# Optimization experiments

Hardware: AMD Instinct MI355X
Metric: run time of the kernel (lower is better)

## Reference

```python
import jax, jax.numpy as jnp
import numpy as np

L, H, LATENT, DM, DH, FF = 4, 4, 256, 768, 192, 1024
EPS = 1e-6      # fast_transformers RecurrentLinearAttention eps
LN_EPS = 1e-5


def make_pe(d_model=LATENT, max_len=5000):
    pos = np.arange(max_len, dtype=np.float32)[:, None]
    div = np.exp(np.arange(0, d_model, 2, dtype=np.float32) * (-np.log(10000.0) / d_model))
    pe = np.zeros((max_len, d_model), np.float32)
    pe[:, 0::2] = np.sin(pos * div)
    pe[:, 1::2] = np.cos(pos * div)
    return jnp.asarray(pe)

PE = make_pe()


def layer_norm(x, g, b):
    m = x.mean(-1, keepdims=True)
    v = ((x - m) ** 2).mean(-1, keepdims=True)
    return (x - m) * jax.lax.rsqrt(v + LN_EPS) * g + b


def setup_inputs() -> dict:
    key = jax.random.key(0)
    ks = jax.random.split(key, 16)
    bs, nj, nf, T, A, C = 8, 25, 6, 80, 6, 12
    s = 0.02
    return dict(
        x=jax.random.normal(ks[0], (bs, nj, nf, T), jnp.float32),
        y=jax.random.randint(ks[1], (bs, A), 0, C),
        ind_map=jnp.sort(jax.random.randint(ks[2], (T, bs), 0, A), axis=0),
        act_tstamps=jnp.sort(jax.random.randint(ks[3], (bs, A), 1, T + 1), axis=1).at[:, -1].set(T),
        skel_W=jax.random.normal(ks[4], (nj * nf, LATENT), jnp.float32) * s,
        skel_b=jnp.zeros((LATENT,), jnp.float32),
        muQuery=jax.random.normal(ks[5], (C, LATENT), jnp.float32),
        sigmaQuery=jax.random.normal(ks[6], (C, LATENT), jnp.float32),
        Wq=jax.random.normal(ks[7], (L, DM, DM), jnp.float32) * s,
        bq=jnp.zeros((L, DM), jnp.float32),
        Wk=jax.random.normal(ks[8], (L, DM, DM), jnp.float32) * s,
        bk=jnp.zeros((L, DM), jnp.float32),
        Wv=jax.random.normal(ks[9], (L, DM, DM), jnp.float32) * s,
        bv=jnp.zeros((L, DM), jnp.float32),
        Wo=jax.random.normal(ks[10], (L, DM, DM), jnp.float32) * s,
        bo=jnp.zeros((L, DM), jnp.float32),
        W1=jax.random.normal(ks[11], (L, DM, FF), jnp.float32) * s,
        b1=jnp.zeros((L, FF), jnp.float32),
        W2=jax.random.normal(ks[12], (L, FF, DM), jnp.float32) * s,
        b2=jnp.zeros((L, DM), jnp.float32),
        ln1_g=jnp.ones((L, DM), jnp.float32), ln1_b=jnp.zeros((L, DM), jnp.float32),
        ln2_g=jnp.ones((L, DM), jnp.float32), ln2_b=jnp.zeros((L, DM), jnp.float32),
        lnf_g=jnp.ones((DM,), jnp.float32), lnf_b=jnp.zeros((DM,), jnp.float32),
    )


def _fwd(x, y, ind_map, act_tstamps, skel_W, skel_b, muQuery, sigmaQuery,
         Wq, bq, Wk, bk, Wv, bv, Wo, bo, W1, b1, W2, b2,
         ln1_g, ln1_b, ln2_g, ln2_b, lnf_g, lnf_b):
    bs, nj, nf, T = x.shape
    # skeleton embedding: [T, bs, njoints*nfeats] @ W -> [T, bs, LATENT]
    xe = x.transpose(3, 0, 1, 2).reshape(T, bs, nj * nf) @ skel_W + skel_b
    mu_q = muQuery[y]        # [bs, A, LATENT]
    sig_q = sigmaQuery[y]
    barange = jnp.arange(bs)

    @jax.checkpoint
    def step(carry, inputs):
        S, Z = carry                         # [L,bs,H,DH,DH], [L,bs,H,DH]
        t, xt, ind_t = inputs
        cm = mu_q[barange, ind_t]            # gather per-sample current action query
        cs = sig_q[barange, ind_t]
        xseq = jnp.stack([cm, cs, xt], 0)    # [3, bs, LATENT]
        start = jnp.where(t == 0, 0, t + 2)  # PositionalEncoding(last_pos=t, offset=2)
        pe3 = jax.lax.dynamic_slice_in_dim(PE, start, 3, 0)
        xseq = xseq + pe3[:, None, :]
        h = xseq.transpose(1, 0, 2).reshape(bs, 3 * LATENT)  # flatten -> [bs, DM]
        nS, nZ = [], []
        for l in range(L):
            q = (h @ Wq[l] + bq[l]).reshape(bs, H, DH)
            k = (h @ Wk[l] + bk[l]).reshape(bs, H, DH)
            v = (h @ Wv[l] + bv[l]).reshape(bs, H, DH)
            Q = jax.nn.elu(q) + 1.0          # linear-attention feature map
            K = jax.nn.elu(k) + 1.0
            Sl = S[l] + K[..., :, None] * v[..., None, :]   # state update S += k (x) v
            Zl = Z[l] + K
            inv = 1.0 / (jnp.einsum('bhd,bhd->bh', Q, Zl) + EPS)
            att = jnp.einsum('bhd,bhdm,bh->bhm', Q, Sl, inv).reshape(bs, DM)
            h1 = layer_norm(h + att @ Wo[l] + bo[l], ln1_g[l], ln1_b[l])
            ffn = jax.nn.relu(h1 @ W1[l] + b1[l]) @ W2[l] + b2[l]
            h = layer_norm(h1 + ffn, ln2_g[l], ln2_b[l])
            nS.append(Sl); nZ.append(Zl)
        h = layer_norm(h, lnf_g, lnf_b)      # encoder final norm
        return (jnp.stack(nS), jnp.stack(nZ)), h

    S0 = jnp.zeros((L, bs, H, DH, DH), x.dtype)
    Z0 = jnp.zeros((L, bs, H, DH), x.dtype)
    _, finals = jax.lax.scan(step, (S0, Z0), (jnp.arange(T), xe, ind_map))  # finals: [T,bs,DM]
    tsel = jnp.maximum(act_tstamps - 1, 0)                       # [bs, A]
    mu = finals[:, :, :LATENT][tsel, barange[:, None]]           # [bs, A, LATENT]
    logvar = finals[:, :, LATENT:2 * LATENT][tsel, barange[:, None]]
    return mu, logvar


def reference(x, y, ind_map, act_tstamps, skel_W, skel_b, muQuery, sigmaQuery,
              Wq, bq, Wk, bk, Wv, bv, Wo, bo, W1, b1, W2, b2,
              ln1_g, ln1_b, ln2_g, ln2_b, lnf_g, lnf_b):
    return _fwd(x, y, ind_map, act_tstamps, skel_W, skel_b, muQuery, sigmaQuery,
                Wq, bq, Wk, bk, Wv, bv, Wo, bo, W1, b1, W2, b2,
                ln1_g, ln1_b, ln2_g, ln2_b, lnf_g, lnf_b)
```

## Files before the change

### kernel.cpp

```cpp
#include <hip/hip_runtime.h>
#include <math.h>

#define TT 80
#define BS 8
#define NA 6
#define DMODEL 768
#define NH 4
#define DH 192
#define FFD 1024
#define NROWS (TT*BS)
#define NQKV (3*DMODEL)

typedef __bf16 bf16;
typedef __bf16 bf16x8 __attribute__((ext_vector_type(8)));
typedef float  f32x4  __attribute__((ext_vector_type(4)));

__device__ __forceinline__ float block_reduce_sum256(float v, float* sm4) {
#pragma unroll
    for (int off = 32; off > 0; off >>= 1) v += __shfl_down(v, off, 64);
    int lane = threadIdx.x & 63, wid = threadIdx.x >> 6;
    if (lane == 0) sm4[wid] = v;
    __syncthreads();
    float r = sm4[0] + sm4[1] + sm4[2] + sm4[3];
    __syncthreads();
    return r;
}

__global__ __launch_bounds__(256) void embed_k(
        const float* __restrict__ x, const int* __restrict__ y,
        const int* __restrict__ ind_map, const float* __restrict__ skel_W,
        const float* __restrict__ skel_b, const float* __restrict__ muQ,
        const float* __restrict__ sigQ, float* __restrict__ h0,
        bf16* __restrict__ h0b) {
    __shared__ float xrow[152];
    int r = blockIdx.x;
    int t = r >> 3, b = r & 7;
    int c = threadIdx.x;
    if (c < 150) xrow[c] = x[(b * 150 + c) * TT + t];
    __syncthreads();
    float acc = skel_b[c];
    for (int jf = 0; jf < 150; jf++) acc += xrow[jf] * skel_W[jf * 256 + c];
    int ind_t = ind_map[t * 8 + b];
    int yb = y[b * NA + ind_t];
    float cm = muQ[yb * 256 + c];
    float cs = sigQ[yb * 256 + c];
    int start = (t == 0) ? 0 : (t + 2);
    float div = expf((float)(c & ~1) * (-9.210340371976184f / 256.0f));
    float p0, p1, p2;
    if (c & 1) {
        p0 = cosf((float)start * div);
        p1 = cosf((float)(start + 1) * div);
        p2 = cosf((float)(start + 2) * div);
    } else {
        p0 = sinf((float)start * div);
        p1 = sinf((float)(start + 1) * div);
        p2 = sinf((float)(start + 2) * div);
    }
    float* hr = h0 + (size_t)r * DMODEL;
    float v0 = cm + p0, v1 = cs + p1, v2 = acc + p2;
    hr[c] = v0; hr[c + 256] = v1; hr[c + 512] = v2;
    bf16* hb = h0b + (size_t)r * DMODEL;
    hb[c] = (bf16)v0; hb[c + 256] = (bf16)v1; hb[c + 512] = (bf16)v2;
}

__global__ __launch_bounds__(256) void transpose_k(
        const float* __restrict__ wq, const float* __restrict__ wk,
        const float* __restrict__ wv, const float* __restrict__ wo,
        const float* __restrict__ w1, const float* __restrict__ w2,
        bf16* __restrict__ qkvT, bf16* __restrict__ woT,
        bf16* __restrict__ w1T, bf16* __restrict__ w2T) {
    int z = blockIdx.z;
    int K = (z == 3) ? 1024 : 768;
    int N = (z == 0) ? 2304 : (z == 2) ? 1024 : 768;
    int k0 = blockIdx.x * 32, n0 = blockIdx.y * 32;
    if (k0 >= K || n0 >= N) return;
    const float* src; bf16* dst; int ldsrc; int ncol;
    if (z == 0) {
        if (n0 < 768)       { src = wq; ncol = n0; }
        else if (n0 < 1536) { src = wk; ncol = n0 - 768; }
        else                { src = wv; ncol = n0 - 1536; }
        dst = qkvT; ldsrc = 768;
    } else if (z == 1) { src = wo; dst = woT; ldsrc = 768;  ncol = n0; }
    else if (z == 2)   { src = w1; dst = w1T; ldsrc = 1024; ncol = n0; }
    else               { src = w2; dst = w2T; ldsrc = 768;  ncol = n0; }
    __shared__ float tile[32][33];
    int tx = threadIdx.x & 31, ty = threadIdx.x >> 5;
#pragma unroll
    for (int i = 0; i < 4; i++) {
        int r = ty + 8 * i;
        tile[r][tx] = src[(size_t)(k0 + r) * ldsrc + ncol + tx];
    }
    __syncthreads();
#pragma unroll
    for (int i = 0; i < 4; i++) {
        int r = ty + 8 * i;
        dst[(size_t)(n0 + r) * K + k0 + tx] = (bf16)tile[tx][r];
    }
}

template <int EPI>
__global__ __launch_bounds__(256) void gemm_mfma(
        const bf16* __restrict__ A, const bf16* __restrict__ Bt,
        const float* __restrict__ bias_q, const float* __restrict__ bias_k,
        const float* __restrict__ bias_v, const float* __restrict__ resid,
        float* __restrict__ outF, bf16* __restrict__ outB,
        int M, int N, int K) {
    __shared__ __attribute__((aligned(16))) bf16 As[64][40];
    __shared__ __attribute__((aligned(16))) bf16 Bs[64][40];
    int tid = threadIdx.x;
    int m0 = blockIdx.y * 64, n0 = blockIdx.x * 64;
    int w = tid >> 6;
    int l = tid & 63;
    int lm = l & 15, lq = l >> 4;
    int sr = tid >> 2;
    int sk = (tid & 3) * 8;
    f32x4 acc[4] = {};
    for (int k0 = 0; k0 < K; k0 += 32) {
        uint4 av = *(const uint4*)&A[(size_t)(m0 + sr) * K + k0 + sk];
        uint4 bv = *(const uint4*)&Bt[(size_t)(n0 + sr) * K + k0 + sk];
        __syncthreads();
        *(uint4*)&As[sr][sk] = av;
        *(uint4*)&Bs[sr][sk] = bv;
        __syncthreads();
        bf16x8 af = *(bf16x8*)&As[w * 16 + lm][lq * 8];
#pragma unroll
        for (int nb = 0; nb < 4; nb++) {
            bf16x8 bfr = *(bf16x8*)&Bs[nb * 16 + lm][lq * 8];
            acc[nb] = __builtin_amdgcn_mfma_f32_16x16x32_bf16(af, bfr, acc[nb], 0, 0, 0);
        }
    }
#pragma unroll
    for (int nb = 0; nb < 4; nb++) {
        int col = n0 + nb * 16 + lm;
        float b;
        bool do_elu = false;
        if (EPI == 0) {
            if (col < 768)       { b = bias_q[col];        do_elu = true; }
            else if (col < 1536) { b = bias_k[col - 768];  do_elu = true; }
            else                 { b = bias_v[col - 1536]; }
        } else {
            b = bias_q[col];
        }
#pragma unroll
        for (int r = 0; r < 4; r++) {
            int row = m0 + w * 16 + lq * 4 + r;
            float v = acc[nb][r] + b;
            if (EPI == 0) {
                if (do_elu) v = (v > 0.0f) ? (v + 1.0f) : expf(v);
                outB[(size_t)row * N + col] = (bf16)v;
            } else if (EPI == 1) {
                v += resid[(size_t)row * N + col];
                outF[(size_t)row * N + col] = v;
            } else {
                v = fmaxf(v, 0.0f);
                outB[(size_t)row * N + col] = (bf16)v;
            }
        }
    }
}

__global__ __launch_bounds__(256) void ln_k(
        const float* __restrict__ in, float* __restrict__ outF,
        bf16* __restrict__ outB,
        const float* __restrict__ g, const float* __restrict__ b) {
    __shared__ float sm4[4];
    int row = blockIdx.x;
    const float* xr = in + (size_t)row * DMODEL;
    int c = threadIdx.x;
    float x0 = xr[c], x1 = xr[c + 256], x2 = xr[c + 512];
    float m = block_reduce_sum256(x0 + x1 + x2, sm4) * (1.0f / 768.0f);
    float d0 = x0 - m, d1 = x1 - m, d2 = x2 - m;
    float v = block_reduce_sum256(d0 * d0 + d1 * d1 + d2 * d2, sm4) * (1.0f / 768.0f);
    float r = rsqrtf(v + 1e-5f);
    float o0 = d0 * r * g[c] + b[c];
    float o1 = d1 * r * g[c + 256] + b[c + 256];
    float o2 = d2 * r * g[c + 512] + b[c + 512];
    float* orow = outF + (size_t)row * DMODEL;
    orow[c] = o0; orow[c + 256] = o1; orow[c + 512] = o2;
    bf16* brow = outB + (size_t)row * DMODEL;
    brow[c] = (bf16)o0; brow[c + 256] = (bf16)o1; brow[c + 512] = (bf16)o2;
}

__global__ __launch_bounds__(320) void attn_k(
        const bf16* __restrict__ qkvB, bf16* __restrict__ att) {
    __shared__ __attribute__((aligned(16))) char smem[64000];
    bf16* Qs = (bf16*)smem;
    bf16* Ks = (bf16*)(smem + 32000);
    bf16* Aij = (bf16*)smem;
    bf16* VT = (bf16*)(smem + 16640);

    int b = blockIdx.x >> 2, h = blockIdx.x & 3;
    int tid = threadIdx.x;
    int w = tid >> 6, l = tid & 63;
    int lm = l & 15, lq = l >> 4;

    uint4 vreg[6];
#pragma unroll
    for (int u = 0; u < 6; u++) {
        int c = tid + 320 * u;
        int t = c / 24, cc = c % 24;
        int d0 = cc * 8;
        size_t g = (size_t)(t * 8 + b) * NQKV + h * DH + d0;
        uint4 qv = *(const uint4*)&qkvB[g];
        uint4 kv = *(const uint4*)&qkvB[g + 768];
        vreg[u]  = *(const uint4*)&qkvB[g + 1536];
        *(uint4*)&Qs[t * 200 + d0] = qv;
        *(uint4*)&Ks[t * 200 + d0] = kv;
    }
    __syncthreads();

    f32x4 acc[5] = {};
#pragma unroll
    for (int k0 = 0; k0 < 192; k0 += 32) {
        bf16x8 af = *(bf16x8*)&Qs[(w * 16 + lm) * 200 + lq * 8 + k0];
#pragma unroll
        for (int nb = 0; nb < 5; nb++) {
            bf16x8 bfr = *(bf16x8*)&Ks[(nb * 16 + lm) * 200 + lq * 8 + k0];
            acc[nb] = __builtin_amdgcn_mfma_f32_16x16x32_bf16(af, bfr, acc[nb], 0, 0, 0);
        }
    }
    float mval[5][4];
    float rs[4] = {0.f, 0.f, 0.f, 0.f};
#pragma unroll
    for (int nb = 0; nb < 5; nb++)
#pragma unroll
        for (int r = 0; r < 4; r++) {
            int t = w * 16 + lq * 4 + r, tau = nb * 16 + lm;
            float v = (tau <= t) ? acc[nb][r] : 0.0f;
            mval[nb][r] = v;
            rs[r] += v;
        }
#pragma unroll
    for (int mk = 1; mk < 16; mk <<= 1)
#pragma unroll
        for (int r = 0; r < 4; r++) rs[r] += __shfl_xor(rs[r], mk, 64);
    float inv[4];
#pragma unroll
    for (int r = 0; r < 4; r++) inv[r] = 1.0f / (rs[r] + 1e-6f);

    __syncthreads();

#pragma unroll
    for (int nb = 0; nb < 5; nb++)
#pragma unroll
        for (int r = 0; r < 4; r++)
            Aij[(w * 16 + lq * 4 + r) * 104 + nb * 16 + lm] = (bf16)mval[nb][r];
    *(uint2*)&Aij[(tid >> 2) * 104 + 80 + (tid & 3) * 4] = make_uint2(0u, 0u);
#pragma unroll
    for (int u = 0; u < 6; u++) {
        int c = tid + 320 * u;
        int t = c / 24, cc = c % 24;
        int d0 = cc * 8;
        bf16 tmp8[8];
        *(uint4*)tmp8 = vreg[u];
#pragma unroll
        for (int j = 0; j < 8; j++) VT[(d0 + j) * 104 + t] = tmp8[j];
    }
    if (tid < 192) {
        *(uint4*)&VT[tid * 104 + 80] = make_uint4(0u, 0u, 0u, 0u);
        *(uint4*)&VT[tid * 104 + 88] = make_uint4(0u, 0u, 0u, 0u);
    }
    __syncthreads();

#pragma unroll 1
    for (int nc = 0; nc < 12; nc++) {
        f32x4 a2 = {};
#pragma unroll
        for (int k0 = 0; k0 < 96; k0 += 32) {
            bf16x8 af = *(bf16x8*)&Aij[(w * 16 + lm) * 104 + lq * 8 + k0];
            bf16x8 bfr = *(bf16x8*)&VT[(nc * 16 + lm) * 104 + lq * 8 + k0];
            a2 = __builtin_amdgcn_mfma_f32_16x16x32_bf16(af, bfr, a2, 0, 0, 0);
        }
#pragma unroll
        for (int r = 0; r < 4; r++) {
            int t = w * 16 + lq * 4 + r;
            att[(size_t)(t * 8 + b) * DMODEL + h * DH + nc * 16 + lm] =
                (bf16)(a2[r] * inv[r]);
        }
    }
}

__global__ __launch_bounds__(256) void final_k(
        const float* __restrict__ h, const int* __restrict__ act_ts,
        const float* __restrict__ g, const float* __restrict__ bb,
        float* __restrict__ out) {
    __shared__ float sm4[4];
    int ba = blockIdx.x;
    int b = ba / NA;
    int ts = act_ts[ba];
    int t = ts - 1; if (t < 0) t = 0;
    const float* xr = h + (size_t)(t * 8 + b) * DMODEL;
    int c = threadIdx.x;
    float x0 = xr[c], x1 = xr[c + 256], x2 = xr[c + 512];
    float m = block_reduce_sum256(x0 + x1 + x2, sm4) * (1.0f / 768.0f);
    float d0 = x0 - m, d1 = x1 - m, d2 = x2 - m;
    float v = block_reduce_sum256(d0 * d0 + d1 * d1 + d2 * d2, sm4) * (1.0f / 768.0f);
    float r = rsqrtf(v + 1e-5f);
    out[ba * 256 + c]            = d0 * r * g[c] + bb[c];
    out[48 * 256 + ba * 256 + c] = d1 * r * g[c + 256] + bb[c + 256];
}

extern "C" void kernel_launch(void* const* d_in, const int* in_sizes, int n_in,
                              void* d_out, int out_size, void* d_ws, size_t ws_size,
                              hipStream_t stream) {
    const float* x       = (const float*)d_in[0];
    const int*   y       = (const int*)d_in[1];
    const int*   ind_map = (const int*)d_in[2];
    const int*   act_ts  = (const int*)d_in[3];
    const float* skel_W  = (const float*)d_in[4];
    const float* skel_b  = (const float*)d_in[5];
    const float* muQ     = (const float*)d_in[6];
    const float* sigQ    = (const float*)d_in[7];
    const float* Wq = (const float*)d_in[8];   const float* bq = (const float*)d_in[9];
    const float* Wk = (const float*)d_in[10];  const float* bk = (const float*)d_in[11];
    const float* Wv = (const float*)d_in[12];  const float* bv = (const float*)d_in[13];
    const float* Wo = (const float*)d_in[14];  const float* bo = (const float*)d_in[15];
    const float* W1 = (const float*)d_in[16];  const float* b1 = (const float*)d_in[17];
    const float* W2 = (const float*)d_in[18];  const float* b2 = (const float*)d_in[19];
    const float* ln1_g = (const float*)d_in[20]; const float* ln1_b = (const float*)d_in[21];
    const float* ln2_g = (const float*)d_in[22]; const float* ln2_b = (const float*)d_in[23];
    const float* lnf_g = (const float*)d_in[24]; const float* lnf_b = (const float*)d_in[25];
    float* out = (float*)d_out;

    char* p = (char*)d_ws;
    const size_t R  = (size_t)NROWS * DMODEL;
    float* h    = (float*)p; p += R * 4;
    float* h1   = (float*)p; p += R * 4;
    float* tmp  = (float*)p; p += R * 4;
    bf16* qkvB  = (bf16*)p;  p += (size_t)NROWS * NQKV * 2;
    bf16* hB    = (bf16*)p;  p += R * 2;
    bf16* h1B   = (bf16*)p;  p += R * 2;
    bf16* attB  = (bf16*)p;  p += R * 2;
    bf16* ffn1B = (bf16*)p;  p += (size_t)NROWS * FFD * 2;
    bf16* qkvT  = (bf16*)p;  p += (size_t)NQKV * DMODEL * 2;
    bf16* woT   = (bf16*)p;  p += (size_t)DMODEL * DMODEL * 2;
    bf16* w1T   = (bf16*)p;  p += (size_t)FFD * DMODEL * 2;
    bf16* w2T   = (bf16*)p;  p += (size_t)DMODEL * FFD * 2;

    embed_k<<<NROWS, 256, 0, stream>>>(x, y, ind_map, skel_W, skel_b, muQ, sigQ, h, hB);

    dim3 gT(32, 72, 4);
    dim3 gQKV(NQKV / 64, 10);
    dim3 g768(12, 10);
    dim3 g1024(16, 10);
    for (int l = 0; l < 4; l++) {
        const float* wq = Wq + (size_t)l * DMODEL * DMODEL;
        const float* wk = Wk + (size_t)l * DMODEL * DMODEL;
        const float* wv = Wv + (size_t)l * DMODEL * DMODEL;
        const float* wo = Wo + (size_t)l * DMODEL * DMODEL;
        const float* w1 = W1 + (size_t)l * DMODEL * FFD;
        const float* w2 = W2 + (size_t)l * FFD * DMODEL;
        transpose_k<<<gT, 256, 0, stream>>>(wq, wk, wv, wo, w1, w2, qkvT, woT, w1T, w2T);
        gemm_mfma<0><<<gQKV, 256, 0, stream>>>(hB, qkvT,
                bq + l * DMODEL, bk + l * DMODEL, bv + l * DMODEL,
                nullptr, nullptr, qkvB, NROWS, NQKV, DMODEL);
        attn_k<<<32, 320, 0, stream>>>(qkvB, attB);
        gemm_mfma<1><<<g768, 256, 0, stream>>>(attB, woT,
                bo + l * DMODEL, nullptr, nullptr, h, tmp, nullptr,
                NROWS, DMODEL, DMODEL);
        ln_k<<<NROWS, 256, 0, stream>>>(tmp, h1, h1B, ln1_g + l * DMODEL, ln1_b + l * DMODEL);
        gemm_mfma<2><<<g1024, 256, 0, stream>>>(h1B, w1T,
                b1 + l * FFD, nullptr, nullptr, nullptr, nullptr, ffn1B,
                NROWS, FFD, DMODEL);
        gemm_mfma<1><<<g768, 256, 0, stream>>>(ffn1B, w2T,
                b2 + l * DMODEL, nullptr, nullptr, h1, tmp, nullptr,
                NROWS, DMODEL, FFD);
        ln_k<<<NROWS, 256, 0, stream>>>(tmp, h, hB, ln2_g + l * DMODEL, ln2_b + l * DMODEL);
    }

    final_k<<<48, 256, 0, stream>>>(h, act_ts, lnf_g, lnf_b, out);
}
```

Measured before the change: 453.3 us.

## Batch weight transposes, prefetch GEMM tiles, use wave-per-row layer norm

All four layers' weights are now transposed to bf16 in one launch before the layer loop, instead of one transpose launch per layer. This removes three launches and lets the transpose overlap with nothing else on the critical path, at the cost of a four times larger weight workspace. The GEMM kernel now stages 64-wide K chunks through two LDS buffers and issues the next chunk's global loads before the MFMAs, overlapping memory latency with compute. Layer norm now processes one row per wave using float4 loads and shuffle reductions, which removes the block-level syncs.

```diff
diff --git a/kernel.cpp b/kernel.cpp
--- a/kernel.cpp
+++ b/kernel.cpp
@@ -64,25 +64,26 @@
 }
 
 __global__ __launch_bounds__(256) void transpose_k(
-        const float* __restrict__ wq, const float* __restrict__ wk,
-        const float* __restrict__ wv, const float* __restrict__ wo,
-        const float* __restrict__ w1, const float* __restrict__ w2,
+        const float* __restrict__ Wq, const float* __restrict__ Wk,
+        const float* __restrict__ Wv, const float* __restrict__ Wo,
+        const float* __restrict__ W1, const float* __restrict__ W2,
         bf16* __restrict__ qkvT, bf16* __restrict__ woT,
         bf16* __restrict__ w1T, bf16* __restrict__ w2T) {
-    int z = blockIdx.z;
+    int lz = blockIdx.z;
+    int l = lz >> 2, z = lz & 3;
     int K = (z == 3) ? 1024 : 768;
     int N = (z == 0) ? 2304 : (z == 2) ? 1024 : 768;
     int k0 = blockIdx.x * 32, n0 = blockIdx.y * 32;
     if (k0 >= K || n0 >= N) return;
     const float* src; bf16* dst; int ldsrc; int ncol;
     if (z == 0) {
-        if (n0 < 768)       { src = wq; ncol = n0; }
-        else if (n0 < 1536) { src = wk; ncol = n0 - 768; }
-        else                { src = wv; ncol = n0 - 1536; }
-        dst = qkvT; ldsrc = 768;
-    } else if (z == 1) { src = wo; dst = woT; ldsrc = 768;  ncol = n0; }
-    else if (z == 2)   { src = w1; dst = w1T; ldsrc = 1024; ncol = n0; }
-    else               { src = w2; dst = w2T; ldsrc = 768;  ncol = n0; }
+        if (n0 < 768)       { src = Wq + (size_t)l * 768 * 768; ncol = n0; }
+        else if (n0 < 1536) { src = Wk + (size_t)l * 768 * 768; ncol = n0 - 768; }
+        else                { src = Wv + (size_t)l * 768 * 768; ncol = n0 - 1536; }
+        dst = qkvT + (size_t)l * NQKV * DMODEL; ldsrc = 768;
+    } else if (z == 1) { src = Wo + (size_t)l * 768 * 768;  dst = woT + (size_t)l * 768 * 768;  ldsrc = 768;  ncol = n0; }
+    else if (z == 2)   { src = W1 + (size_t)l * 768 * 1024; dst = w1T + (size_t)l * 1024 * 768; ldsrc = 1024; ncol = n0; }
+    else               { src = W2 + (size_t)l * 1024 * 768; dst = w2T + (size_t)l * 768 * 1024; ldsrc = 768;  ncol = n0; }
     __shared__ float tile[32][33];
     int tx = threadIdx.x & 31, ty = threadIdx.x >> 5;
 #pragma unroll
@@ -105,8 +106,10 @@
         const float* __restrict__ bias_v, const float* __restrict__ resid,
         float* __restrict__ outF, bf16* __restrict__ outB,
         int M, int N, int K) {
-    __shared__ __attribute__((aligned(16))) bf16 As[64][40];
-    __shared__ __attribute__((aligned(16))) bf16 Bs[64][40];
+    __shared__ __attribute__((aligned(16))) bf16 As0[64][40];
+    __shared__ __attribute__((aligned(16))) bf16 As1[64][40];
+    __shared__ __attribute__((aligned(16))) bf16 Bs0[64][40];
+    __shared__ __attribute__((aligned(16))) bf16 Bs1[64][40];
     int tid = threadIdx.x;
     int m0 = blockIdx.y * 64, n0 = blockIdx.x * 64;
     int w = tid >> 6;
@@ -114,19 +117,36 @@
     int lm = l & 15, lq = l >> 4;
     int sr = tid >> 2;
     int sk = (tid & 3) * 8;
+    const bf16* Arow = &A[(size_t)(m0 + sr) * K];
+    const bf16* Brow = &Bt[(size_t)(n0 + sr) * K];
     f32x4 acc[4] = {};
-    for (int k0 = 0; k0 < K; k0 += 32) {
-        uint4 av = *(const uint4*)&A[(size_t)(m0 + sr) * K + k0 + sk];
-        uint4 bv = *(const uint4*)&Bt[(size_t)(n0 + sr) * K + k0 + sk];
+    uint4 a0 = *(const uint4*)&Arow[sk];
+    uint4 a1 = *(const uint4*)&Arow[32 + sk];
+    uint4 b0 = *(const uint4*)&Brow[sk];
+    uint4 b1 = *(const uint4*)&Brow[32 + sk];
+    for (int k0 = 0; k0 < K; k0 += 64) {
         __syncthreads();
-        *(uint4*)&As[sr][sk] = av;
-        *(uint4*)&Bs[sr][sk] = bv;
+        *(uint4*)&As0[sr][sk] = a0;
+        *(uint4*)&As1[sr][sk] = a1;
+        *(uint4*)&Bs0[sr][sk] = b0;
+        *(uint4*)&Bs1[sr][sk] = b1;
         __syncthreads();
-        bf16x8 af = *(bf16x8*)&As[w * 16 + lm][lq * 8];
+        int k2 = k0 + 64; if (k2 >= K) k2 = 0;
+        a0 = *(const uint4*)&Arow[k2 + sk];
+        a1 = *(const uint4*)&Arow[k2 + 32 + sk];
+        b0 = *(const uint4*)&Brow[k2 + sk];
+        b1 = *(const uint4*)&Brow[k2 + 32 + sk];
+        bf16x8 af0 = *(bf16x8*)&As0[w * 16 + lm][lq * 8];
+        bf16x8 af1 = *(bf16x8*)&As1[w * 16 + lm][lq * 8];
 #pragma unroll
         for (int nb = 0; nb < 4; nb++) {
-            bf16x8 bfr = *(bf16x8*)&Bs[nb * 16 + lm][lq * 8];
-            acc[nb] = __builtin_amdgcn_mfma_f32_16x16x32_bf16(af, bfr, acc[nb], 0, 0, 0);
+            bf16x8 bf0 = *(bf16x8*)&Bs0[nb * 16 + lm][lq * 8];
+            acc[nb] = __builtin_amdgcn_mfma_f32_16x16x32_bf16(af0, bf0, acc[nb], 0, 0, 0);
+        }
+#pragma unroll
+        for (int nb = 0; nb < 4; nb++) {
+            bf16x8 bf1 = *(bf16x8*)&Bs1[nb * 16 + lm][lq * 8];
+            acc[nb] = __builtin_amdgcn_mfma_f32_16x16x32_bf16(af1, bf1, acc[nb], 0, 0, 0);
         }
     }
 #pragma unroll
@@ -163,22 +183,43 @@
         const float* __restrict__ in, float* __restrict__ outF,
         bf16* __restrict__ outB,
         const float* __restrict__ g, const float* __restrict__ b) {
-    __shared__ float sm4[4];
-    int row = blockIdx.x;
+    int wave = threadIdx.x >> 6, lane = threadIdx.x & 63;
+    int row = blockIdx.x * 4 + wave;
     const float* xr = in + (size_t)row * DMODEL;
-    int c = threadIdx.x;
-    float x0 = xr[c], x1 = xr[c + 256], x2 = xr[c + 512];
-    float m = block_reduce_sum256(x0 + x1 + x2, sm4) * (1.0f / 768.0f);
-    float d0 = x0 - m, d1 = x1 - m, d2 = x2 - m;
-    float v = block_reduce_sum256(d0 * d0 + d1 * d1 + d2 * d2, sm4) * (1.0f / 768.0f);
-    float r = rsqrtf(v + 1e-5f);
-    float o0 = d0 * r * g[c] + b[c];
-    float o1 = d1 * r * g[c + 256] + b[c + 256];
-    float o2 = d2 * r * g[c + 512] + b[c + 512];
+    float4 v[3];
+    float s = 0.0f;
+#pragma unroll
+    for (int j = 0; j < 3; j++) {
+        v[j] = *(const float4*)&xr[lane * 4 + 256 * j];
+        s += v[j].x + v[j].y + v[j].z + v[j].w;
+    }
+#pragma unroll
+    for (int mk = 1; mk < 64; mk <<= 1) s += __shfl_xor(s, mk, 64);
+    float m = s * (1.0f / 768.0f);
+    float sq = 0.0f;
+#pragma unroll
+    for (int j = 0; j < 3; j++) {
+        v[j].x -= m; v[j].y -= m; v[j].z -= m; v[j].w -= m;
+        sq += v[j].x * v[j].x + v[j].y * v[j].y + v[j].z * v[j].z + v[j].w * v[j].w;
+    }
+#pragma unroll
+    for (int mk = 1; mk < 64; mk <<= 1) sq += __shfl_xor(sq, mk, 64);
+    float r = rsqrtf(sq * (1.0f / 768.0f) + 1e-5f);
     float* orow = outF + (size_t)row * DMODEL;
-    orow[c] = o0; orow[c + 256] = o1; orow[c + 512] = o2;
     bf16* brow = outB + (size_t)row * DMODEL;
-    brow[c] = (bf16)o0; brow[c + 256] = (bf16)o1; brow[c + 512] = (bf16)o2;
+#pragma unroll
+    for (int j = 0; j < 3; j++) {
+        int c = lane * 4 + 256 * j;
+        float4 gg = *(const float4*)&g[c];
+        float4 bb = *(const float4*)&b[c];
+        float o0 = v[j].x * r * gg.x + bb.x;
+        float o1 = v[j].y * r * gg.y + bb.y;
+        float o2 = v[j].z * r * gg.z + bb.z;
+        float o3 = v[j].w * r * gg.w + bb.w;
+        *(float4*)&orow[c] = make_float4(o0, o1, o2, o3);
+        bf16 tmp4[4] = {(bf16)o0, (bf16)o1, (bf16)o2, (bf16)o3};
+        *(uint2*)&brow[c] = *(uint2*)tmp4;
+    }
 }
 
 __global__ __launch_bounds__(320) void attn_k(
@@ -332,40 +373,38 @@
     bf16* h1B   = (bf16*)p;  p += R * 2;
     bf16* attB  = (bf16*)p;  p += R * 2;
     bf16* ffn1B = (bf16*)p;  p += (size_t)NROWS * FFD * 2;
-    bf16* qkvT  = (bf16*)p;  p += (size_t)NQKV * DMODEL * 2;
-    bf16* woT   = (bf16*)p;  p += (size_t)DMODEL * DMODEL * 2;
-    bf16* w1T   = (bf16*)p;  p += (size_t)FFD * DMODEL * 2;
-    bf16* w2T   = (bf16*)p;  p += (size_t)DMODEL * FFD * 2;
-
+    bf16* qkvT  = (bf16*)p;  p += (size_t)4 * NQKV * DMODEL * 2;
+    bf16* woT   = (bf16*)p;  p += (size_t)4 * DMODEL * DMODEL * 2;
+    bf16* w1T   = (bf16*)p;  p += (size_t)4 * FFD * DMODEL * 2;
+    bf16* w2T   = (bf16*)p;  p += (size_t)4 * DMODEL * FFD * 2;
+
+    dim3 gT(32, 72, 16);
+    transpose_k<<<gT, 256, 0, stream>>>(Wq, Wk, Wv, Wo, W1, W2, qkvT, woT, w1T, w2T);
     embed_k<<<NROWS, 256, 0, stream>>>(x, y, ind_map, skel_W, skel_b, muQ, sigQ, h, hB);
 
-    dim3 gT(32, 72, 4);
     dim3 gQKV(NQKV / 64, 10);
     dim3 g768(12, 10);
     dim3 g1024(16, 10);
     for (int l = 0; l < 4; l++) {
-        const float* wq = Wq + (size_t)l * DMODEL * DMODEL;
-        const float* wk = Wk + (size_t)l * DMODEL * DMODEL;
-        const float* wv = Wv + (size_t)l * DMODEL * DMODEL;
-        const float* wo = Wo + (size_t)l * DMODEL * DMODEL;
-        const float* w1 = W1 + (size_t)l * DMODEL * FFD;
-        const float* w2 = W2 + (size_t)l * FFD * DMODEL;
-        transpose_k<<<gT, 256, 0, stream>>>(wq, wk, wv, wo, w1, w2, qkvT, woT, w1T, w2T);
-        gemm_mfma<0><<<gQKV, 256, 0, stream>>>(hB, qkvT,
+        const bf16* qkvTl = qkvT + (size_t)l * NQKV * DMODEL;
+        const bf16* woTl  = woT  + (size_t)l * DMODEL * DMODEL;
+        const bf16* w1Tl  = w1T  + (size_t)l * FFD * DMODEL;
+        const bf16* w2Tl  = w2T  + (size_t)l * DMODEL * FFD;
+        gemm_mfma<0><<<gQKV, 256, 0, stream>>>(hB, qkvTl,
                 bq + l * DMODEL, bk + l * DMODEL, bv + l * DMODEL,
                 nullptr, nullptr, qkvB, NROWS, NQKV, DMODEL);
         attn_k<<<32, 320, 0, stream>>>(qkvB, attB);
-        gemm_mfma<1><<<g768, 256, 0, stream>>>(attB, woT,
+        gemm_mfma<1><<<g768, 256, 0, stream>>>(attB, woTl,
                 bo + l * DMODEL, nullptr, nullptr, h, tmp, nullptr,
                 NROWS, DMODEL, DMODEL);
-        ln_k<<<NROWS, 256, 0, stream>>>(tmp, h1, h1B, ln1_g + l * DMODEL, ln1_b + l * DMODEL);
-        gemm_mfma<2><<<g1024, 256, 0, stream>>>(h1B, w1T,
+        ln_k<<<NROWS / 4, 256, 0, stream>>>(tmp, h1, h1B, ln1_g + l * DMODEL, ln1_b + l * DMODEL);
+        gemm_mfma<2><<<g1024, 256, 0, stream>>>(h1B, w1Tl,
                 b1 + l * FFD, nullptr, nullptr, nullptr, nullptr, ffn1B,
                 NROWS, FFD, DMODEL);
-        gemm_mfma<1><<<g768, 256, 0, stream>>>(ffn1B, w2T,
+        gemm_mfma<1><<<g768, 256, 0, stream>>>(ffn1B, w2Tl,
                 b2 + l * DMODEL, nullptr, nullptr, h1, tmp, nullptr,
                 NROWS, DMODEL, FFD);
-        ln_k<<<NROWS, 256, 0, stream>>>(tmp, h, hB, ln2_g + l * DMODEL, ln2_b + l * DMODEL);
+        ln_k<<<NROWS / 4, 256, 0, stream>>>(tmp, h, hB, ln2_g + l * DMODEL, ln2_b + l * DMODEL);
     }
 
     final_k<<<48, 256, 0, stream>>>(h, act_ts, lnf_g, lnf_b, out);
```

New measurement: 422.5 us. 1.07x faster.
